# Kernel tuning notes

Measured on AMD Instinct MI355X. Metric: run time of the kernel, lower is better.

Reference implementation:

```python
import jax, jax.numpy as jnp
import numpy as np

THRESHOLD = 1.0
RESET_VOLTAGE = 0.0

@jax.custom_vjp
def spike(m):
    # Heaviside spike with surrogate gradient 1/(1+10|m-thr|)^2
    return (m > THRESHOLD).astype(m.dtype)

def _spike_fwd(m):
    return spike(m), m

def _spike_bwd(m, g):
    surrogate = 1.0 / (1.0 + 10.0 * jnp.abs(m - THRESHOLD)) ** 2
    return (g * surrogate,)

spike.defvjp(_spike_fwd, _spike_bwd)


def setup_inputs() -> dict:
    key = jax.random.key(0)
    k1, k2 = jax.random.split(key)
    B, I, O, T = 128, 2048, 2048, 100
    spike_input = (jax.random.uniform(k1, (B, I, T)) < 0.1).astype(jnp.float32)
    weight = jax.random.normal(k2, (I, O), dtype=jnp.float32) * 0.1
    return {"spike_input": spike_input, "weight": weight}


def reference(spike_input, weight):
    # Batch the input-current matmul once across all T timesteps: [T, B, O]
    currents = jnp.einsum('bit,io->tbo', spike_input, weight)

    def step(membrane, cur):
        membrane = membrane + cur
        fired = spike(membrane)
        membrane = membrane * (1.0 - fired) + RESET_VOLTAGE * fired
        return membrane, fired

    B, O = currents.shape[1], currents.shape[2]
    init = jnp.zeros((B, O), dtype=currents.dtype)
    _, fires = jax.lax.scan(step, init, currents)  # fires: [T, B, O]
    return jnp.transpose(fires, (1, 2, 0))  # [B, O, T]
```

## Files before the change

### kernel.cpp

```cpp
#include <hip/hip_runtime.h>
#include <stdint.h>

#define B_ 128
#define I_ 2048
#define O_ 2048
#define T_ 100
#define TAU 2e-4f

typedef short bf16x8 __attribute__((ext_vector_type(8)));
typedef float f32x4 __attribute__((ext_vector_type(4)));

#define WT_BYTES  ((size_t)3 * O_ * I_ * 2)
#define ST_BYTES  ((size_t)B_ * T_ * I_ * 2)
#define CNT_OFF   (WT_BYTES + ST_BYTES)
#define WL_OFF    (CNT_OFF + 256)
#define WL_MAX    ((size_t)B_ * O_)
#define WS_NEED   (WL_OFF + WL_MAX * 4)

__device__ __forceinline__ unsigned short f2bf(float x) {
    uint32_t u = __float_as_uint(x);
    uint32_t r = (u + 0x7fffu + ((u >> 16) & 1u)) >> 16;
    return (unsigned short)r;
}
__device__ __forceinline__ float bf2f(unsigned short h) {
    return __uint_as_float(((uint32_t)h) << 16);
}

__global__ void init_cnt(unsigned* cnt) { if (threadIdx.x == 0) cnt[0] = 0u; }

__global__ void prep_w(const float* __restrict__ W, unsigned short* __restrict__ Wt) {
    __shared__ float tile[64][65];
    const int tid = threadIdx.x;
    const int ib = (blockIdx.x & 31) * 64;
    const int ob = (blockIdx.x >> 5) * 64;
#pragma unroll
    for (int k = 0; k < 4; ++k) {
        int flat4 = k * 256 + tid;
        int row = flat4 >> 4, c4 = flat4 & 15;
        float4 v = *(const float4*)&W[(size_t)(ib + row) * O_ + ob + c4 * 4];
        tile[row][c4 * 4 + 0] = v.x; tile[row][c4 * 4 + 1] = v.y;
        tile[row][c4 * 4 + 2] = v.z; tile[row][c4 * 4 + 3] = v.w;
    }
    __syncthreads();
#pragma unroll
    for (int k = 0; k < 4; ++k) {
        int flat = k * 256 + tid;
        int o = flat >> 4, i4 = flat & 15;
        unsigned short h[3][4];
#pragma unroll
        for (int jj = 0; jj < 4; ++jj) {
            float wv = tile[i4 * 4 + jj][o];
            unsigned short h0 = f2bf(wv); float r = wv - bf2f(h0);
            unsigned short h1 = f2bf(r);  r = r - bf2f(h1);
            unsigned short h2 = f2bf(r);
            h[0][jj] = h0; h[1][jj] = h1; h[2][jj] = h2;
        }
        size_t base = (size_t)(ob + o) * I_ + ib + i4 * 4;
#pragma unroll
        for (int p = 0; p < 3; ++p) {
            ushort4 v4 = make_ushort4(h[p][0], h[p][1], h[p][2], h[p][3]);
            *(ushort4*)(Wt + (size_t)p * O_ * I_ + base) = v4;
        }
    }
}

__global__ void prep_s(const float* __restrict__ S, unsigned short* __restrict__ St) {
    __shared__ float tile[128][101];
    const int tid = threadIdx.x;
    const int b  = blockIdx.x >> 4;
    const int ib = (blockIdx.x & 15) * 128;
    for (int k = 0; k < 13; ++k) {
        int flat4 = k * 256 + tid;
        if (flat4 < 3200) {
            int row = flat4 / 25, c4 = flat4 % 25;
            float4 v = *(const float4*)&S[((size_t)b * I_ + ib + row) * T_ + c4 * 4];
            tile[row][c4 * 4 + 0] = v.x; tile[row][c4 * 4 + 1] = v.y;
            tile[row][c4 * 4 + 2] = v.z; tile[row][c4 * 4 + 3] = v.w;
        }
    }
    __syncthreads();
    for (int k = 0; k < 13; ++k) {
        int flat = k * 256 + tid;
        if (flat < 3200) {
            int t = flat >> 5, i4 = flat & 31;
            ushort4 v;
            v.x = f2bf(tile[i4 * 4 + 0][t]); v.y = f2bf(tile[i4 * 4 + 1][t]);
            v.z = f2bf(tile[i4 * 4 + 2][t]); v.w = f2bf(tile[i4 * 4 + 3][t]);
            *(ushort4*)(St + ((size_t)b * T_ + t) * I_ + ib + i4 * 4) = v;
        }
    }
}

__device__ __forceinline__ void compute_tile(const char* smem, int lane, int w,
                                             f32x4 acc[7][2]) {
    const int c = lane & 15, kg = lane >> 4;
    bf16x8 a[7];
#pragma unroll
    for (int mt = 0; mt < 7; ++mt) {
        int R = mt * 16 + c;
        a[mt] = *(const bf16x8*)(smem + R * 64 + ((kg ^ ((R >> 1) & 3)) * 16));
    }
#pragma unroll
    for (int p = 0; p < 3; ++p) {
#pragma unroll
        for (int nt = 0; nt < 2; ++nt) {
            int R = w * 32 + nt * 16 + c;
            bf16x8 bv = *(const bf16x8*)(smem + 7168 + p * 16384 + R * 64 +
                                         ((kg ^ ((R >> 1) & 3)) * 16));
#pragma unroll
            for (int mt = 0; mt < 7; ++mt)
                acc[mt][nt] = __builtin_amdgcn_mfma_f32_16x16x32_bf16(
                    a[mt], bv, acc[mt][nt], 0, 0, 0);
        }
    }
}

__launch_bounds__(512, 4)
__global__ void lif_mfma3(const unsigned short* __restrict__ Wt_,
                          const unsigned short* __restrict__ St_,
                          float* __restrict__ out,
                          unsigned* __restrict__ cnt,
                          unsigned* __restrict__ wl) {
    __shared__ f32x4 smem4[59392 / 16];
    char* smem = (char*)smem4;
    const char* Wt = (const char*)Wt_;
    const char* St = (const char*)St_;
    const int tid = threadIdx.x, lane = tid & 63, w = tid >> 6;

    const int bid = blockIdx.x;
    const int x = bid & 7, j = bid >> 3;
    const int oc = j >> 4;
    const int b  = x * 16 + (j & 15);
    const int o0 = oc * 256;

    f32x4 acc[7][2];
#pragma unroll
    for (int mt = 0; mt < 7; ++mt)
#pragma unroll
        for (int nt = 0; nt < 2; ++nt)
            acc[mt][nt] = (f32x4){0.f, 0.f, 0.f, 0.f};

    if (tid < 48) *(f32x4*)(smem + 6400 + tid * 16) = (f32x4){0.f, 0.f, 0.f, 0.f};

    const size_t I2 = I_ * 2;
    const size_t PLANE = (size_t)O_ * I_ * 2;

    for (int kt = 0; kt < 64; ++kt) {
        __syncthreads();
        if (tid < 400) {
            int r = tid >> 2, kc = tid & 3;
            f32x4 v = *(const f32x4*)(St + ((size_t)b * T_ + r) * I2 + kt * 64 + kc * 16);
            *(f32x4*)(smem + r * 64 + ((kc ^ ((r >> 1) & 3)) * 16)) = v;
        }
#pragma unroll
        for (int s = 0; s < 6; ++s) {
            int q = s * 512 + tid;
            int r = q >> 2, kc = q & 3;
            int p = r >> 8, ol = r & 255;
            f32x4 v = *(const f32x4*)(Wt + (size_t)p * PLANE +
                                      (size_t)(o0 + ol) * I2 + kt * 64 + kc * 16);
            *(f32x4*)(smem + 7168 + p * 16384 + ol * 64 +
                      ((kc ^ ((ol >> 1) & 3)) * 16)) = v;
        }
        __syncthreads();
        compute_tile(smem, lane, w, acc);
    }
    __syncthreads();

    const int c = lane & 15, kg = lane >> 4;
    for (int ph = 0; ph < 2; ++ph) {
        if ((w >> 2) == ph) {
            float* Cw = (float*)(smem + (w & 3) * 14848);
#pragma unroll
            for (int mt = 0; mt < 7; ++mt)
#pragma unroll
                for (int nt = 0; nt < 2; ++nt)
#pragma unroll
                    for (int r = 0; r < 4; ++r)
                        Cw[(nt * 16 + c) * 116 + mt * 16 + kg * 4 + r] = acc[mt][nt][r];
        }
        __syncthreads();
        if ((w >> 2) == ph && lane < 32) {
            float* row = (float*)(smem + (w & 3) * 14848) + lane * 116;
            float m = 0.f;
            bool flag = false;
            for (int t = 0; t < T_; ++t) {
                m += row[t];
                float d = m - 1.0f;
                flag |= (fabsf(d) < TAU);
                bool f = d > 0.0f;
                row[t] = f ? 1.0f : 0.0f;
                m = f ? 0.0f : m;
            }
            if (flag) {
                unsigned o = (unsigned)(o0 + ph * 128 + (w & 3) * 32 + lane);
                unsigned idx = atomicAdd(cnt, 1u);
                wl[idx] = ((unsigned)b << 11) | o;
            }
        }
        __syncthreads();
        float* ob = out + ((size_t)b * O_ + o0 + ph * 128) * T_;
        for (int k = 0; k < 7; ++k) {
            int f4 = k * 512 + tid;
            if (f4 < 3200) {
                int o = f4 / 25, t4 = f4 % 25;
                f32x4 v = *(const f32x4*)((const float*)(smem + (o >> 5) * 14848) +
                                          (o & 31) * 116 + t4 * 4);
                *(f32x4*)(ob + (size_t)o * T_ + t4 * 4) = v;
            }
        }
        __syncthreads();
    }
}

__launch_bounds__(256, 2)
__global__ void fixup(const float* __restrict__ spike,
                      const float* __restrict__ W,
                      float* __restrict__ out,
                      const unsigned* __restrict__ cnt,
                      const unsigned* __restrict__ wl) {
    __shared__ float Wcol[I_];
    __shared__ float cbuf[T_];
    const unsigned n = cnt[0];
    for (unsigned ri = blockIdx.x; ri < n; ri += gridDim.x) {
        unsigned e = wl[ri];
        const int b = (int)(e >> 11), o = (int)(e & 2047u);
#pragma unroll
        for (int k = 0; k < 8; ++k)
            Wcol[k * 256 + threadIdx.x] = W[(size_t)(k * 256 + threadIdx.x) * O_ + o];
        __syncthreads();
        const int t = threadIdx.x;
        if (t < T_) {
            float c = 0.f;
            const float* srow = spike + (size_t)b * I_ * T_ + t;
            for (int i = 0; i < I_; ++i)
                c = fmaf(Wcol[i], srow[(size_t)i * T_], c);
            cbuf[t] = c;
        }
        __syncthreads();
        if (threadIdx.x == 0) {
            float m = 0.f;
            float* orow = out + ((size_t)b * O_ + o) * T_;
            for (int t2 = 0; t2 < T_; ++t2) {
                m += cbuf[t2];
                bool f = m > 1.0f;
                orow[t2] = f ? 1.0f : 0.0f;
                m = f ? 0.0f : m;
            }
        }
        __syncthreads();
    }
}

#define TI 32
#define TO 256
__launch_bounds__(256, 3)
__global__ void lif_fused_kernel(const float* __restrict__ spike,
                                 const float* __restrict__ weight,
                                 float* __restrict__ out) {
    __shared__ float Wlds[TI][TO];
    __shared__ float Slds[TI][128];
    __shared__ float m_buf[TO];
    const int tid = threadIdx.x;
    const int lane = tid & 63;
    const int tq = tid >> 6;
    const int b = blockIdx.x >> 3;
    const int oc = blockIdx.x & 7;
    const int o0 = oc * TO;
    float4 acc[25];
#pragma unroll
    for (int t = 0; t < 25; ++t) acc[t] = make_float4(0.f, 0.f, 0.f, 0.f);
    const float4* Wf4 = (const float4*)weight;
    for (int it = 0; it < I_ / TI; ++it) {
        const int i0 = it * TI;
        __syncthreads();
#pragma unroll
        for (int k = 0; k < 8; ++k) {
            int flat4 = k * 256 + tid;
            int i_l = flat4 >> 6, o4 = flat4 & 63;
            float4 v = Wf4[(size_t)(i0 + i_l) * (O_ / 4) + (o0 >> 2) + o4];
            ((float4*)Wlds)[i_l * (TO / 4) + o4] = v;
        }
#pragma unroll
        for (int k = 0; k < 13; ++k) {
            int flat = k * 256 + tid;
            if (flat < TI * T_) {
                int i_l = flat / T_, t = flat - i_l * T_;
                int q = t / 25, tt = t - q * 25;
                Slds[i_l][q * 32 + tt] = spike[((size_t)b * I_ + i0 + i_l) * T_ + t];
            }
        }
        __syncthreads();
        for (int i_l = 0; i_l < TI; ++i_l) {
            float4 wv = ((const float4*)Wlds)[i_l * (TO / 4) + lane];
            const float* srow = &Slds[i_l][tq * 32];
#pragma unroll
            for (int v = 0; v < 6; ++v) {
                float4 sv = ((const float4*)srow)[v];
                acc[v*4+0].x = fmaf(wv.x, sv.x, acc[v*4+0].x); acc[v*4+0].y = fmaf(wv.y, sv.x, acc[v*4+0].y);
                acc[v*4+0].z = fmaf(wv.z, sv.x, acc[v*4+0].z); acc[v*4+0].w = fmaf(wv.w, sv.x, acc[v*4+0].w);
                acc[v*4+1].x = fmaf(wv.x, sv.y, acc[v*4+1].x); acc[v*4+1].y = fmaf(wv.y, sv.y, acc[v*4+1].y);
                acc[v*4+1].z = fmaf(wv.z, sv.y, acc[v*4+1].z); acc[v*4+1].w = fmaf(wv.w, sv.y, acc[v*4+1].w);
                acc[v*4+2].x = fmaf(wv.x, sv.z, acc[v*4+2].x); acc[v*4+2].y = fmaf(wv.y, sv.z, acc[v*4+2].y);
                acc[v*4+2].z = fmaf(wv.z, sv.z, acc[v*4+2].z); acc[v*4+2].w = fmaf(wv.w, sv.z, acc[v*4+2].w);
                acc[v*4+3].x = fmaf(wv.x, sv.w, acc[v*4+3].x); acc[v*4+3].y = fmaf(wv.y, sv.w, acc[v*4+3].y);
                acc[v*4+3].z = fmaf(wv.z, sv.w, acc[v*4+3].z); acc[v*4+3].w = fmaf(wv.w, sv.w, acc[v*4+3].w);
            }
            float s24 = srow[24];
            acc[24].x = fmaf(wv.x, s24, acc[24].x); acc[24].y = fmaf(wv.y, s24, acc[24].y);
            acc[24].z = fmaf(wv.z, s24, acc[24].z); acc[24].w = fmaf(wv.w, s24, acc[24].w);
        }
    }
    __syncthreads();
    for (int r = 0; r < 4; ++r) {
        if (tq == r) {
#pragma unroll
            for (int jj = 0; jj < 4; ++jj) {
                const int ol = lane * 4 + jj;
                float m = (r == 0) ? 0.0f : m_buf[ol];
                float* orow = out + ((size_t)b * O_ + o0 + ol) * T_ + r * 25;
#pragma unroll
                for (int t = 0; t < 25; ++t) {
                    float cu = (jj == 0) ? acc[t].x : (jj == 1) ? acc[t].y
                             : (jj == 2) ? acc[t].z : acc[t].w;
                    m += cu;
                    bool f = (m > 1.0f);
                    orow[t] = f ? 1.0f : 0.0f;
                    m = f ? 0.0f : m;
                }
                m_buf[ol] = m;
            }
        }
        __syncthreads();
    }
}

extern "C" void kernel_launch(void* const* d_in, const int* in_sizes, int n_in,
                              void* d_out, int out_size, void* d_ws, size_t ws_size,
                              hipStream_t stream) {
    const float* spike  = (const float*)d_in[0];
    const float* weight = (const float*)d_in[1];
    float* out = (float*)d_out;

    if (ws_size < WS_NEED) {
        lif_fused_kernel<<<dim3(B_ * (O_ / TO)), dim3(256), 0, stream>>>(spike, weight, out);
        return;
    }
    unsigned short* Wt = (unsigned short*)d_ws;
    unsigned short* St = (unsigned short*)((char*)d_ws + WT_BYTES);
    unsigned* cnt = (unsigned*)((char*)d_ws + CNT_OFF);
    unsigned* wl  = (unsigned*)((char*)d_ws + WL_OFF);

    init_cnt<<<dim3(1), dim3(64), 0, stream>>>(cnt);
    prep_w<<<dim3((I_ / 64) * (O_ / 64)), dim3(256), 0, stream>>>(weight, Wt);
    prep_s<<<dim3(B_ * (I_ / 128)), dim3(256), 0, stream>>>(spike, St);
    lif_mfma3<<<dim3(B_ * (O_ / 256)), dim3(512), 0, stream>>>(Wt, St, out, cnt, wl);
    fixup<<<dim3(2048), dim3(256), 0, stream>>>(spike, weight, out, cnt, wl);
}
```

Baseline: 602.5 us.

## Drop third bf16 weight plane from MFMA, widen fixup tolerance, fold init into prep

The main MFMA kernel now multiplies against only two of the three bf16 split planes of the weight, cutting its weight loads and MFMA work by a third. To make up for the lost precision, the threshold-closeness tolerance grows fivefold, so more (batch, output) pairs are sent to the exact fixup pass. The fixup rebuilds the weight column from the three bf16 planes instead of strided fp32 reads, and the counter reset is folded into prep_w to save a launch. The trade-off is a larger fixup workload, and the reconstructed weight may not be bit-identical to the fp32 original.

Result: slower. 920.5 us (+52.8%).

```diff
diff --git a/kernel.cpp b/kernel.cpp
--- a/kernel.cpp
+++ b/kernel.cpp
@@ -5,7 +5,7 @@
 #define I_ 2048
 #define O_ 2048
 #define T_ 100
-#define TAU 2e-4f
+#define TAU 1e-3f
 
 typedef short bf16x8 __attribute__((ext_vector_type(8)));
 typedef float f32x4 __attribute__((ext_vector_type(4)));
@@ -26,11 +26,11 @@
     return __uint_as_float(((uint32_t)h) << 16);
 }
 
-__global__ void init_cnt(unsigned* cnt) { if (threadIdx.x == 0) cnt[0] = 0u; }
-
-__global__ void prep_w(const float* __restrict__ W, unsigned short* __restrict__ Wt) {
+__global__ void prep_w(const float* __restrict__ W, unsigned short* __restrict__ Wt,
+                       unsigned* __restrict__ cnt) {
     __shared__ float tile[64][65];
     const int tid = threadIdx.x;
+    if (blockIdx.x == 0 && tid == 0) cnt[0] = 0u;
     const int ib = (blockIdx.x & 31) * 64;
     const int ob = (blockIdx.x >> 5) * 64;
 #pragma unroll
@@ -101,7 +101,7 @@
         a[mt] = *(const bf16x8*)(smem + R * 64 + ((kg ^ ((R >> 1) & 3)) * 16));
     }
 #pragma unroll
-    for (int p = 0; p < 3; ++p) {
+    for (int p = 0; p < 2; ++p) {
 #pragma unroll
         for (int nt = 0; nt < 2; ++nt) {
             int R = w * 32 + nt * 16 + c;
@@ -116,7 +116,7 @@
 }
 
 __launch_bounds__(512, 4)
-__global__ void lif_mfma3(const unsigned short* __restrict__ Wt_,
+__global__ void lif_mfma4(const unsigned short* __restrict__ Wt_,
                           const unsigned short* __restrict__ St_,
                           float* __restrict__ out,
                           unsigned* __restrict__ cnt,
@@ -153,7 +153,7 @@
             *(f32x4*)(smem + r * 64 + ((kc ^ ((r >> 1) & 3)) * 16)) = v;
         }
 #pragma unroll
-        for (int s = 0; s < 6; ++s) {
+        for (int s = 0; s < 4; ++s) {
             int q = s * 512 + tid;
             int r = q >> 2, kc = q & 3;
             int p = r >> 8, ol = r & 255;
@@ -214,20 +214,30 @@
 }
 
 __launch_bounds__(256, 2)
-__global__ void fixup(const float* __restrict__ spike,
-                      const float* __restrict__ W,
+__global__ void fixup(const unsigned short* __restrict__ Wt,
+                      const float* __restrict__ spike,
                       float* __restrict__ out,
                       const unsigned* __restrict__ cnt,
                       const unsigned* __restrict__ wl) {
     __shared__ float Wcol[I_];
     __shared__ float cbuf[T_];
     const unsigned n = cnt[0];
+    const size_t PLANE = (size_t)O_ * I_;
     for (unsigned ri = blockIdx.x; ri < n; ri += gridDim.x) {
         unsigned e = wl[ri];
         const int b = (int)(e >> 11), o = (int)(e & 2047u);
 #pragma unroll
-        for (int k = 0; k < 8; ++k)
-            Wcol[k * 256 + threadIdx.x] = W[(size_t)(k * 256 + threadIdx.x) * O_ + o];
+        for (int k = 0; k < 2; ++k) {
+            int i4 = k * 256 + threadIdx.x;
+            size_t base = (size_t)o * I_ + i4 * 4;
+            ushort4 a0 = *(const ushort4*)(Wt + 0 * PLANE + base);
+            ushort4 a1 = *(const ushort4*)(Wt + 1 * PLANE + base);
+            ushort4 a2 = *(const ushort4*)(Wt + 2 * PLANE + base);
+            Wcol[i4 * 4 + 0] = (bf2f(a0.x) + bf2f(a1.x)) + bf2f(a2.x);
+            Wcol[i4 * 4 + 1] = (bf2f(a0.y) + bf2f(a1.y)) + bf2f(a2.y);
+            Wcol[i4 * 4 + 2] = (bf2f(a0.z) + bf2f(a1.z)) + bf2f(a2.z);
+            Wcol[i4 * 4 + 3] = (bf2f(a0.w) + bf2f(a1.w)) + bf2f(a2.w);
+        }
         __syncthreads();
         const int t = threadIdx.x;
         if (t < T_) {
@@ -351,9 +361,8 @@
     unsigned* cnt = (unsigned*)((char*)d_ws + CNT_OFF);
     unsigned* wl  = (unsigned*)((char*)d_ws + WL_OFF);
 
-    init_cnt<<<dim3(1), dim3(64), 0, stream>>>(cnt);
-    prep_w<<<dim3((I_ / 64) * (O_ / 64)), dim3(256), 0, stream>>>(weight, Wt);
+    prep_w<<<dim3((I_ / 64) * (O_ / 64)), dim3(256), 0, stream>>>(weight, Wt, cnt);
     prep_s<<<dim3(B_ * (I_ / 128)), dim3(256), 0, stream>>>(spike, St);
-    lif_mfma3<<<dim3(B_ * (O_ / 256)), dim3(512), 0, stream>>>(Wt, St, out, cnt, wl);
-    fixup<<<dim3(2048), dim3(256), 0, stream>>>(spike, weight, out, cnt, wl);
-}
+    lif_mfma4<<<dim3(B_ * (O_ / 256)), dim3(512), 0, stream>>>(Wt, St, out, cnt, wl);
+    fixup<<<dim3(2048), dim3(256), 0, stream>>>(Wt, spike, out, cnt, wl);
+}
```

## Drop third bf16 weight plane and fold threshold fixup into MFMA kernel

Applied to the files above, without the earlier changes.

The MFMA matmul now uses two bf16 split planes of the weight instead of three. This removes a third of the MFMA work and of the weight-tile loads. To absorb the larger rounding error, the near-threshold tolerance is widened. Flagged neurons are then recomputed inside the same block from a shared-memory list, so the separate global worklist, counter-init kernel and fixup kernel are gone. The two prep kernels are also merged into a single launch. The risks are a serial recompute tail in blocks that flag many neurons, and silent loss of flags once more than 256 are recorded in one block.

Measured after the change: 746.1 us. 1.24x slower.

```diff
diff --git a/kernel.cpp b/kernel.cpp
--- a/kernel.cpp
+++ b/kernel.cpp
@@ -5,17 +5,14 @@
 #define I_ 2048
 #define O_ 2048
 #define T_ 100
-#define TAU 2e-4f
+#define TAU 5e-4f
 
 typedef short bf16x8 __attribute__((ext_vector_type(8)));
 typedef float f32x4 __attribute__((ext_vector_type(4)));
 
 #define WT_BYTES  ((size_t)3 * O_ * I_ * 2)
 #define ST_BYTES  ((size_t)B_ * T_ * I_ * 2)
-#define CNT_OFF   (WT_BYTES + ST_BYTES)
-#define WL_OFF    (CNT_OFF + 256)
-#define WL_MAX    ((size_t)B_ * O_)
-#define WS_NEED   (WL_OFF + WL_MAX * 4)
+#define WS_NEED   (WT_BYTES + ST_BYTES)
 
 __device__ __forceinline__ unsigned short f2bf(float x) {
     uint32_t u = __float_as_uint(x);
@@ -26,67 +23,65 @@
     return __uint_as_float(((uint32_t)h) << 16);
 }
 
-__global__ void init_cnt(unsigned* cnt) { if (threadIdx.x == 0) cnt[0] = 0u; }
-
-__global__ void prep_w(const float* __restrict__ W, unsigned short* __restrict__ Wt) {
-    __shared__ float tile[64][65];
+__global__ void prep_all(const float* __restrict__ W, const float* __restrict__ S,
+                         unsigned short* __restrict__ Wt, unsigned short* __restrict__ St) {
+    __shared__ float tile[128 * 101];
     const int tid = threadIdx.x;
-    const int ib = (blockIdx.x & 31) * 64;
-    const int ob = (blockIdx.x >> 5) * 64;
-#pragma unroll
-    for (int k = 0; k < 4; ++k) {
-        int flat4 = k * 256 + tid;
-        int row = flat4 >> 4, c4 = flat4 & 15;
-        float4 v = *(const float4*)&W[(size_t)(ib + row) * O_ + ob + c4 * 4];
-        tile[row][c4 * 4 + 0] = v.x; tile[row][c4 * 4 + 1] = v.y;
-        tile[row][c4 * 4 + 2] = v.z; tile[row][c4 * 4 + 3] = v.w;
-    }
-    __syncthreads();
-#pragma unroll
-    for (int k = 0; k < 4; ++k) {
-        int flat = k * 256 + tid;
-        int o = flat >> 4, i4 = flat & 15;
-        unsigned short h[3][4];
-#pragma unroll
-        for (int jj = 0; jj < 4; ++jj) {
-            float wv = tile[i4 * 4 + jj][o];
-            unsigned short h0 = f2bf(wv); float r = wv - bf2f(h0);
-            unsigned short h1 = f2bf(r);  r = r - bf2f(h1);
-            unsigned short h2 = f2bf(r);
-            h[0][jj] = h0; h[1][jj] = h1; h[2][jj] = h2;
-        }
-        size_t base = (size_t)(ob + o) * I_ + ib + i4 * 4;
-#pragma unroll
-        for (int p = 0; p < 3; ++p) {
-            ushort4 v4 = make_ushort4(h[p][0], h[p][1], h[p][2], h[p][3]);
-            *(ushort4*)(Wt + (size_t)p * O_ * I_ + base) = v4;
-        }
-    }
-}
-
-__global__ void prep_s(const float* __restrict__ S, unsigned short* __restrict__ St) {
-    __shared__ float tile[128][101];
-    const int tid = threadIdx.x;
-    const int b  = blockIdx.x >> 4;
-    const int ib = (blockIdx.x & 15) * 128;
-    for (int k = 0; k < 13; ++k) {
-        int flat4 = k * 256 + tid;
-        if (flat4 < 3200) {
-            int row = flat4 / 25, c4 = flat4 % 25;
-            float4 v = *(const float4*)&S[((size_t)b * I_ + ib + row) * T_ + c4 * 4];
-            tile[row][c4 * 4 + 0] = v.x; tile[row][c4 * 4 + 1] = v.y;
-            tile[row][c4 * 4 + 2] = v.z; tile[row][c4 * 4 + 3] = v.w;
-        }
-    }
-    __syncthreads();
-    for (int k = 0; k < 13; ++k) {
-        int flat = k * 256 + tid;
-        if (flat < 3200) {
-            int t = flat >> 5, i4 = flat & 31;
-            ushort4 v;
-            v.x = f2bf(tile[i4 * 4 + 0][t]); v.y = f2bf(tile[i4 * 4 + 1][t]);
-            v.z = f2bf(tile[i4 * 4 + 2][t]); v.w = f2bf(tile[i4 * 4 + 3][t]);
-            *(ushort4*)(St + ((size_t)b * T_ + t) * I_ + ib + i4 * 4) = v;
+    if (blockIdx.x < 1024) {
+        const int ib = (blockIdx.x & 31) * 64;
+        const int ob = (blockIdx.x >> 5) * 64;
+#pragma unroll
+        for (int k = 0; k < 4; ++k) {
+            int flat4 = k * 256 + tid;
+            int row = flat4 >> 4, c4 = flat4 & 15;
+            float4 v = *(const float4*)&W[(size_t)(ib + row) * O_ + ob + c4 * 4];
+            tile[row * 65 + c4 * 4 + 0] = v.x; tile[row * 65 + c4 * 4 + 1] = v.y;
+            tile[row * 65 + c4 * 4 + 2] = v.z; tile[row * 65 + c4 * 4 + 3] = v.w;
+        }
+        __syncthreads();
+#pragma unroll
+        for (int k = 0; k < 4; ++k) {
+            int flat = k * 256 + tid;
+            int o = flat >> 4, i4 = flat & 15;
+            unsigned short h[3][4];
+#pragma unroll
+            for (int jj = 0; jj < 4; ++jj) {
+                float wv = tile[(i4 * 4 + jj) * 65 + o];
+                unsigned short h0 = f2bf(wv); float r = wv - bf2f(h0);
+                unsigned short h1 = f2bf(r);  r = r - bf2f(h1);
+                unsigned short h2 = f2bf(r);
+                h[0][jj] = h0; h[1][jj] = h1; h[2][jj] = h2;
+            }
+            size_t base = (size_t)(ob + o) * I_ + ib + i4 * 4;
+#pragma unroll
+            for (int p = 0; p < 3; ++p) {
+                ushort4 v4 = make_ushort4(h[p][0], h[p][1], h[p][2], h[p][3]);
+                *(ushort4*)(Wt + (size_t)p * O_ * I_ + base) = v4;
+            }
+        }
+    } else {
+        const int bid2 = blockIdx.x - 1024;
+        const int b  = bid2 >> 4;
+        const int ib = (bid2 & 15) * 128;
+        for (int k = 0; k < 13; ++k) {
+            int flat4 = k * 256 + tid;
+            if (flat4 < 3200) {
+                int row = flat4 / 25, c4 = flat4 % 25;
+                float4 v = *(const float4*)&S[((size_t)b * I_ + ib + row) * T_ + c4 * 4];
+                tile[row * 101 + c4 * 4 + 0] = v.x; tile[row * 101 + c4 * 4 + 1] = v.y;
+                tile[row * 101 + c4 * 4 + 2] = v.z; tile[row * 101 + c4 * 4 + 3] = v.w;
+            }
+        }
+        __syncthreads();
+        for (int k = 0; k < 13; ++k) {
+            int flat = k * 256 + tid;
+            if (flat < 3200) {
+                int t = flat >> 5, i4 = flat & 31;
+                ushort4 v;
+                v.x = f2bf(tile[(i4 * 4 + 0) * 101 + t]); v.y = f2bf(tile[(i4 * 4 + 1) * 101 + t]);
+                v.z = f2bf(tile[(i4 * 4 + 2) * 101 + t]); v.w = f2bf(tile[(i4 * 4 + 3) * 101 + t]);
+                *(ushort4*)(St + ((size_t)b * T_ + t) * I_ + ib + i4 * 4) = v;
+            }
         }
     }
 }
@@ -101,7 +96,7 @@
         a[mt] = *(const bf16x8*)(smem + R * 64 + ((kg ^ ((R >> 1) & 3)) * 16));
     }
 #pragma unroll
-    for (int p = 0; p < 3; ++p) {
+    for (int p = 0; p < 2; ++p) {
 #pragma unroll
         for (int nt = 0; nt < 2; ++nt) {
             int R = w * 32 + nt * 16 + c;
@@ -116,12 +111,12 @@
 }
 
 __launch_bounds__(512, 4)
-__global__ void lif_mfma3(const unsigned short* __restrict__ Wt_,
+__global__ void lif_mfma5(const unsigned short* __restrict__ Wt_,
                           const unsigned short* __restrict__ St_,
-                          float* __restrict__ out,
-                          unsigned* __restrict__ cnt,
-                          unsigned* __restrict__ wl) {
+                          float* __restrict__ out) {
     __shared__ f32x4 smem4[59392 / 16];
+    __shared__ unsigned fl_list[256];
+    __shared__ unsigned fl_n;
     char* smem = (char*)smem4;
     const char* Wt = (const char*)Wt_;
     const char* St = (const char*)St_;
@@ -140,6 +135,7 @@
         for (int nt = 0; nt < 2; ++nt)
             acc[mt][nt] = (f32x4){0.f, 0.f, 0.f, 0.f};
 
+    if (tid == 0) fl_n = 0u;
     if (tid < 48) *(f32x4*)(smem + 6400 + tid * 16) = (f32x4){0.f, 0.f, 0.f, 0.f};
 
     const size_t I2 = I_ * 2;
@@ -153,7 +149,7 @@
             *(f32x4*)(smem + r * 64 + ((kc ^ ((r >> 1) & 3)) * 16)) = v;
         }
 #pragma unroll
-        for (int s = 0; s < 6; ++s) {
+        for (int s = 0; s < 4; ++s) {
             int q = s * 512 + tid;
             int r = q >> 2, kc = q & 3;
             int p = r >> 8, ol = r & 255;
@@ -194,8 +190,8 @@
             }
             if (flag) {
                 unsigned o = (unsigned)(o0 + ph * 128 + (w & 3) * 32 + lane);
-                unsigned idx = atomicAdd(cnt, 1u);
-                wl[idx] = ((unsigned)b << 11) | o;
+                unsigned idx = atomicAdd(&fl_n, 1u);
+                if (idx < 256u) fl_list[idx] = o;
             }
         }
         __syncthreads();
@@ -211,40 +207,45 @@
         }
         __syncthreads();
     }
-}
-
-__launch_bounds__(256, 2)
-__global__ void fixup(const float* __restrict__ spike,
-                      const float* __restrict__ W,
-                      float* __restrict__ out,
-                      const unsigned* __restrict__ cnt,
-                      const unsigned* __restrict__ wl) {
-    __shared__ float Wcol[I_];
-    __shared__ float cbuf[T_];
-    const unsigned n = cnt[0];
-    for (unsigned ri = blockIdx.x; ri < n; ri += gridDim.x) {
-        unsigned e = wl[ri];
-        const int b = (int)(e >> 11), o = (int)(e & 2047u);
-#pragma unroll
-        for (int k = 0; k < 8; ++k)
-            Wcol[k * 256 + threadIdx.x] = W[(size_t)(k * 256 + threadIdx.x) * O_ + o];
-        __syncthreads();
-        const int t = threadIdx.x;
-        if (t < T_) {
-            float c = 0.f;
-            const float* srow = spike + (size_t)b * I_ * T_ + t;
-            for (int i = 0; i < I_; ++i)
-                c = fmaf(Wcol[i], srow[(size_t)i * T_], c);
-            cbuf[t] = c;
-        }
-        __syncthreads();
-        if (threadIdx.x == 0) {
+
+    const unsigned n = fl_n;
+    if (n == 0u) return;
+    float* Wcol = (float*)smem;
+    float* cbuf = (float*)(smem + 8192);
+    const size_t PLANE_E = (size_t)O_ * I_;
+    for (unsigned ri = 0; ri < n; ++ri) {
+        const int o = (int)fl_list[ri];
+        {
+            size_t base = (size_t)o * I_ + tid * 4;
+            ushort4 a0 = *(const ushort4*)(Wt_ + 0 * PLANE_E + base);
+            ushort4 a1 = *(const ushort4*)(Wt_ + 1 * PLANE_E + base);
+            ushort4 a2 = *(const ushort4*)(Wt_ + 2 * PLANE_E + base);
+            Wcol[tid * 4 + 0] = (bf2f(a0.x) + bf2f(a1.x)) + bf2f(a2.x);
+            Wcol[tid * 4 + 1] = (bf2f(a0.y) + bf2f(a1.y)) + bf2f(a2.y);
+            Wcol[tid * 4 + 2] = (bf2f(a0.z) + bf2f(a1.z)) + bf2f(a2.z);
+            Wcol[tid * 4 + 3] = (bf2f(a0.w) + bf2f(a1.w)) + bf2f(a2.w);
+        }
+        __syncthreads();
+        if (tid < T_) {
+            const ushort4* srow = (const ushort4*)(St_ + ((size_t)b * T_ + tid) * I_);
+            float cc = 0.f;
+            for (int i4 = 0; i4 < I_ / 4; ++i4) {
+                ushort4 s4 = srow[i4];
+                cc = fmaf(Wcol[i4 * 4 + 0], bf2f(s4.x), cc);
+                cc = fmaf(Wcol[i4 * 4 + 1], bf2f(s4.y), cc);
+                cc = fmaf(Wcol[i4 * 4 + 2], bf2f(s4.z), cc);
+                cc = fmaf(Wcol[i4 * 4 + 3], bf2f(s4.w), cc);
+            }
+            cbuf[tid] = cc;
+        }
+        __syncthreads();
+        if (tid == 0) {
             float m = 0.f;
             float* orow = out + ((size_t)b * O_ + o) * T_;
-            for (int t2 = 0; t2 < T_; ++t2) {
-                m += cbuf[t2];
+            for (int t = 0; t < T_; ++t) {
+                m += cbuf[t];
                 bool f = m > 1.0f;
-                orow[t2] = f ? 1.0f : 0.0f;
+                orow[t] = f ? 1.0f : 0.0f;
                 m = f ? 0.0f : m;
             }
         }
@@ -348,12 +349,7 @@
     }
     unsigned short* Wt = (unsigned short*)d_ws;
     unsigned short* St = (unsigned short*)((char*)d_ws + WT_BYTES);
-    unsigned* cnt = (unsigned*)((char*)d_ws + CNT_OFF);
-    unsigned* wl  = (unsigned*)((char*)d_ws + WL_OFF);
-
-    init_cnt<<<dim3(1), dim3(64), 0, stream>>>(cnt);
-    prep_w<<<dim3((I_ / 64) * (O_ / 64)), dim3(256), 0, stream>>>(weight, Wt);
-    prep_s<<<dim3(B_ * (I_ / 128)), dim3(256), 0, stream>>>(spike, St);
-    lif_mfma3<<<dim3(B_ * (O_ / 256)), dim3(512), 0, stream>>>(Wt, St, out, cnt, wl);
-    fixup<<<dim3(2048), dim3(256), 0, stream>>>(spike, weight, out, cnt, wl);
-}
+
+    prep_all<<<dim3(3072), dim3(256), 0, stream>>>(weight, spike, Wt, St);
+    lif_mfma5<<<dim3(B_ * (O_ / 256)), dim3(512), 0, stream>>>(Wt, St, out);
+}
```
